# Kernel optimization log

Hardware: AMD Instinct MI355X
Metric: run time of the kernel (lower is better)

The kernel has to match this reference:

```python
import jax, jax.numpy as jnp
from jax import lax
import numpy as np
import math

KSIZE, STRIDE, RATE, FUSE_K, SCALE, FUSE = 3, 1, 2, 3, 10.0, True
DN = ('NCHW', 'OIHW', 'NCHW')


def extract_image_patches(img, kernel, stride=1):
    # Faithful to the torch helper, including the F.pad quirk where pad_row
    # (computed from height) is applied to the width axis and vice versa.
    bsz, c, h, w = img.shape
    h2 = math.ceil(h / stride)
    w2 = math.ceil(w / stride)
    pad_row = (h2 - 1) * stride + kernel - h
    pad_col = (w2 - 1) * stride + kernel - w
    x = jnp.pad(img, ((0, 0), (0, 0),
                      (pad_col // 2, pad_col - pad_col // 2),
                      (pad_row // 2, pad_row - pad_row // 2)))
    cols = []
    for i in range(kernel):
        for j in range(kernel):
            cols.append(x[:, :, i:i + (h2 - 1) * stride + 1:stride,
                          j:j + (w2 - 1) * stride + 1:stride])
    patches = jnp.stack(cols, axis=-1).reshape(bsz, c, h2, w2, kernel, kernel)
    patches = jnp.transpose(patches, (0, 4, 5, 1, 2, 3))  # [b,kh,kw,c,h2,w2]
    return patches.reshape(bsz, -1, h2, w2)


def setup_inputs() -> dict:
    key = jax.random.key(0)
    k1, k2, k3 = jax.random.split(key, 3)
    f = jax.random.normal(k1, (4, 128, 96, 96), dtype=jnp.float32)
    b = jax.random.normal(k2, (4, 128, 96, 96), dtype=jnp.float32)
    mask = jax.random.uniform(k3, (4, 1, 96, 96), dtype=jnp.float32)
    return {'f': f, 'b': b, 'mask': mask}


def reference(f, b, mask):
    bs, cs, hs, ws = f.shape
    kernel = RATE * 2
    # raw background patches used as conv_transpose filters (C-order reshape as in torch .view)
    raw_w = extract_image_patches(b, kernel, RATE * STRIDE)
    raw_w = raw_w.reshape(bs, -1, kernel, kernel, cs).transpose(0, 1, 4, 2, 3)  # [bs,L,cs,4,4]
    # nearest downsample by rate (matches F.interpolate nearest with scale 1/rate)
    fd = f[:, :, ::RATE, ::RATE]
    bd = b[:, :, ::RATE, ::RATE]
    md = mask[:, :, ::RATE, ::RATE]
    ih, iw = bd.shape[2], bd.shape[3]
    L = ih * iw
    w = extract_image_patches(bd, KSIZE, STRIDE)
    w = w.reshape(bs, -1, KSIZE, KSIZE, cs).transpose(0, 1, 4, 2, 3)  # [bs,L,cs,3,3]
    m = extract_image_patches(md, KSIZE, STRIDE)
    m = m.reshape(bs, -1, 1, KSIZE, KSIZE).transpose(0, 2, 3, 4, 1)  # [bs,1,3,3,L]
    mms = (jnp.mean(1.0 - m, axis=(1, 2, 3)) < 0.85).astype(f.dtype)  # [bs,L]
    fuse_w = jnp.eye(FUSE_K, dtype=f.dtype).reshape(1, 1, FUSE_K, FUSE_K)

    def per_sample(xi, wi, raw_wi, mm):
        # xi [cs,ih,iw], wi [L,cs,3,3], raw_wi [L,cs,4,4], mm [L]
        norm = jnp.sqrt(jnp.sum(wi * wi, axis=(1, 2, 3)) + 1e-8)
        wi_n = wi / jnp.maximum(norm, 1e-4)[:, None, None, None]
        yi = lax.conv_general_dilated(xi[None], wi_n, (1, 1), ((1, 1), (1, 1)),
                                      dimension_numbers=DN)  # [1,L,ih,iw]
        if FUSE:
            yi = yi.reshape(1, 1, ih * iw, ih * iw)
            yi = lax.conv_general_dilated(yi, fuse_w, (1, 1), ((1, 1), (1, 1)), dimension_numbers=DN)
            yi = yi.reshape(1, ih, iw, ih, iw).transpose(0, 2, 1, 4, 3)
            yi = yi.reshape(1, 1, ih * iw, ih * iw)
            yi = lax.conv_general_dilated(yi, fuse_w, (1, 1), ((1, 1), (1, 1)), dimension_numbers=DN)
            yi = yi.reshape(1, iw, ih, iw, ih).transpose(0, 2, 1, 4, 3)
        yi = yi.reshape(1, ih, iw, iw * ih)
        yi = yi * mm
        yi = jax.nn.softmax(yi * SCALE, axis=3)
        yi = yi * mm
        off = jnp.argmax(yi, axis=3).astype(jnp.int32)
        off = jnp.stack([off // hs, off % hs], axis=-1).transpose(0, 3, 1, 2)  # [1,2,ih,iw]
        yi = yi.transpose(0, 3, 1, 2)  # [1,L,ih,iw]
        # conv_transpose2d(yi, raw_wi, stride=RATE, padding=1) == dilated corr with flipped, transposed kernel
        w_t = jnp.flip(raw_wi, (-2, -1)).transpose(1, 0, 2, 3)  # [cs,L,4,4]
        pad = kernel - 1 - 1
        out = lax.conv_general_dilated(yi, w_t, (1, 1), ((pad, pad), (pad, pad)),
                                       lhs_dilation=(RATE, RATE), dimension_numbers=DN) / 4.0
        return out[0], off[0]

    y, offsets = jax.vmap(per_sample)(fd, w, raw_w, mms)  # y [bs,cs,hs,ws], offsets [bs,2,ih,iw]
    grid = jnp.stack([jnp.broadcast_to(jnp.arange(ih)[:, None], (ih, iw)),
                      jnp.broadcast_to(jnp.arange(iw)[None, :], (ih, iw))], 0).astype(jnp.int32)
    offsets = offsets - grid[None]
    # flow_to_image (external numpy visualization) omitted; raw offsets returned instead.
    return y, offsets
```

## Files before the change

### kernel.cpp

```cpp
#include <hip/hip_runtime.h>
#include <hip/hip_bf16.h>
#include <math.h>

#define IH 48
#define IW 48
#define LTOT 2304
#define CS 128
#define HS 96
#define KRED 1152
#define CRED 2048

typedef unsigned short u16;
typedef __attribute__((ext_vector_type(8))) short short8;
typedef __attribute__((ext_vector_type(8))) unsigned short ushort8;
typedef __attribute__((ext_vector_type(4))) float floatx4;

#define NS    ((size_t)LTOT*LTOT)
#define PLANE ((size_t)LTOT*KRED)

#define OFF_APL  ((size_t)0)
#define OFF_BPL  ((size_t)10616832)
#define OFF_S    ((size_t)21233664)
#define OFF_C    ((size_t)42467328)
#define OFF_SM   ((size_t)61341696)
#define REGION   ((size_t)61360128)

__device__ __forceinline__ u16 f2bf(float v) {
    __hip_bfloat16 h = __float2bfloat16(v);
    return *reinterpret_cast<u16*>(&h);
}
__device__ __forceinline__ float bf2f(u16 b) {
    __hip_bfloat16 h = *reinterpret_cast<__hip_bfloat16*>(&b);
    return __bfloat162float(h);
}
__device__ __forceinline__ void split2(float v, u16& a, u16& b) {
    a = f2bf(v);
    b = f2bf(v - bf2f(a));
}

__global__ __launch_bounds__(256) void k_wgather(const float* __restrict__ b,
                                                 u16* __restrict__ Ag,
                                                 int b0, size_t zsU) {
    int bi = b0 + blockIdx.z;
    u16* A = Ag + (size_t)blockIdx.z * zsU;
    int l = blockIdx.x, t = threadIdx.x;
    __shared__ float red[256];
    float myv[5];
    float ss = 0.f;
#pragma unroll
    for (int k = 0; k < 5; ++k) {
        int G = t + 256 * k;
        float val = 0.f;
        if (G < KRED) {
            int F = l * KRED + G;
            int p2 = F / LTOT, s = F - p2 * LTOT;
            int i = p2 / 384, j = (p2 / 128) % 3, c = p2 & 127;
            int u = s / IW + i - 1, v = s % IW + j - 1;
            if (u >= 0 && u < IH && v >= 0 && v < IW)
                val = b[(((size_t)bi * CS + c) * HS + 2 * u) * HS + 2 * v];
        }
        myv[k] = val;
        ss += val * val;
    }
    red[t] = ss; __syncthreads();
    for (int o = 128; o > 0; o >>= 1) { if (t < o) red[t] += red[t + o]; __syncthreads(); }
    float ninv = 1.0f / fmaxf(sqrtf(red[0] + 1e-8f), 1e-4f);
#pragma unroll
    for (int k = 0; k < 5; ++k) {
        int G = t + 256 * k;
        if (G < KRED) {
            u16 h1, h2; split2(myv[k] * ninv, h1, h2);
            size_t F = (size_t)l * KRED + G;
            A[F] = h1; A[PLANE + F] = h2;
        }
    }
}

__global__ __launch_bounds__(256) void k_gather_x_tiled(const float* __restrict__ f,
                                                        u16* __restrict__ Bg,
                                                        int b0, size_t zsU) {
    __shared__ float ldsf[128 * 55];
    int bi = b0 + blockIdx.z;
    u16* B = Bg + (size_t)blockIdx.z * zsU;
    int bx = blockIdx.x;
    int y = bx / 3, x0 = (bx % 3) * 16;
    int t = threadIdx.x;
    for (int i = 0; i < 27; ++i) {
        int g = i * 256 + t;
        if (g < 6912) {
            int vl = g % 18;
            int row = (g / 18) % 3;
            int c = g / 54;
            int u = y + row - 1;
            int v = x0 - 1 + vl;
            float val = 0.f;
            if (u >= 0 && u < IH && v >= 0 && v < IW)
                val = f[(((size_t)bi * CS + c) * HS + 2 * u) * HS + 2 * v];
            ldsf[c * 55 + row * 18 + vl] = val;
        }
    }
    __syncthreads();
    for (int i = 0; i < 72; ++i) {
        int o = i * 256 + t;
        int xp = o / 1152, G = o - xp * 1152;
        int k1 = G / 384, k2 = (G >> 7) % 3, c = G & 127;
        float val = ldsf[c * 55 + k1 * 18 + xp + k2];
        u16 h1, h2; split2(val, h1, h2);
        size_t idx = (size_t)(y * IW + x0 + xp) * KRED + G;
        B[idx] = h1; B[PLANE + idx] = h2;
    }
}

__global__ __launch_bounds__(256) void k_mm(const float* __restrict__ mask,
                                            float* __restrict__ mmvg, int b0, size_t zsF) {
    int bi = b0 + blockIdx.z;
    float* out = mmvg + (size_t)blockIdx.z * zsF;
    int q = blockIdx.x * 256 + threadIdx.x;
    if (q >= LTOT) return;
    float ssum = 0.f;
    for (int t = 0; t < 9; t++) {
        int F = q * 9 + t;
        int pm = F / LTOT, s = F % LTOT;
        int i = pm / 3, j = pm % 3;
        int u = s / IW + i - 1, v = s % IW + j - 1;
        float val = 0.f;
        if (u >= 0 && u < IH && v >= 0 && v < IW)
            val = mask[((size_t)bi * HS + 2 * u) * HS + 2 * v];
        ssum += 1.0f - val;
    }
    out[q] = (ssum / 9.0f < 0.85f) ? 1.0f : 0.0f;
}

template <int NP, int BK>
__global__ __launch_bounds__(256) void k_gemm_mfma(const u16* __restrict__ Ag,
                                                   const u16* __restrict__ Bg,
                                                   float* __restrict__ Cg,
                                                   size_t zsA, size_t zsB, size_t zsC,
                                                   size_t planeStride,
                                                   int M, int N, int K) {
    constexpr int SLOTS = BK / 8;
    constexpr int SMASK = SLOTS - 1;
    constexpr int TSZ = 128 * BK;
    constexpr int NLD = NP * BK / 16;
    __shared__ u16 lds[2 * NP * TSZ];
    u16* As = lds;
    u16* Bs = lds + NP * TSZ;
    const int tid = threadIdx.x;
    const int lane = tid & 63;
    const int wave = tid >> 6;
    const int wr = (wave >> 1) * 64, wc = (wave & 1) * 64;
    const int lrow = lane & 15, lq = lane >> 4;

    unsigned gx = gridDim.x, gy = gridDim.y;
    unsigned nwg = gx * gy * gridDim.z;
    unsigned wg = (blockIdx.z * gy + blockIdx.y) * gx + blockIdx.x;
    {
        unsigned q = nwg >> 3, r = nwg & 7, xcd = wg & 7, lid = wg >> 3;
        wg = (xcd < r ? xcd * (q + 1) : r * (q + 1) + (xcd - r) * q) + lid;
    }
    unsigned z = wg / (gx * gy);
    unsigned rem2 = wg - z * gx * gy;
    const int bm = (int)(rem2 / gx) * 128, bn = (int)(rem2 % gx) * 128;

    const u16* A = Ag + (size_t)z * zsA;
    const u16* B = Bg + (size_t)z * zsB;
    float* C = Cg + (size_t)z * zsC;

    floatx4 acc[4][4];
#pragma unroll
    for (int i = 0; i < 4; i++)
#pragma unroll
        for (int j = 0; j < 4; j++) acc[i][j] = (floatx4){0.f, 0.f, 0.f, 0.f};

    for (int kt = 0; kt < K; kt += BK) {
        ushort8 stA[NLD], stB[NLD];
#pragma unroll
        for (int e = 0; e < NLD; ++e) {
            int g = e * 256 + tid;
            int p = g / (128 * SLOTS);
            int gg = g % (128 * SLOTS);
            int row = gg / SLOTS, slot = gg & SMASK;
            stA[e] = *(const ushort8*)(A + (size_t)p * planeStride + (size_t)(bm + row) * K + kt + slot * 8);
            stB[e] = *(const ushort8*)(B + (size_t)p * planeStride + (size_t)(bn + row) * K + kt + slot * 8);
        }
        __syncthreads();
#pragma unroll
        for (int e = 0; e < NLD; ++e) {
            int g = e * 256 + tid;
            int p = g / (128 * SLOTS);
            int gg = g % (128 * SLOTS);
            int row = gg / SLOTS, slot = gg & SMASK;
            int dst = p * TSZ + row * BK + ((slot ^ (row & SMASK)) << 3);
            *(ushort8*)&As[dst] = stA[e];
            *(ushort8*)&Bs[dst] = stB[e];
        }
        __syncthreads();

#pragma unroll
        for (int ks = 0; ks < BK / 32; ++ks) {
            short8 af[NP][4];
#pragma unroll
            for (int p = 0; p < NP; ++p)
#pragma unroll
                for (int mi = 0; mi < 4; ++mi) {
                    int row = wr + mi * 16 + lrow;
                    af[p][mi] = *(const short8*)&As[p * TSZ + row * BK + ((((ks << 2) | lq) ^ (row & SMASK)) << 3)];
                }
#pragma unroll
            for (int ni = 0; ni < 4; ++ni) {
                short8 bfr[NP];
                int rowb = wc + ni * 16 + lrow;
                int bslot = ((((ks << 2) | lq) ^ (rowb & SMASK)) << 3);
#pragma unroll
                for (int p = 0; p < NP; ++p)
                    bfr[p] = *(const short8*)&Bs[p * TSZ + rowb * BK + bslot];
#pragma unroll
                for (int mi = 0; mi < 4; ++mi) {
                    if constexpr (NP == 1) {
                        acc[mi][ni] = __builtin_amdgcn_mfma_f32_16x16x32_bf16(af[0][mi], bfr[0], acc[mi][ni], 0, 0, 0);
                    } else {
                        acc[mi][ni] = __builtin_amdgcn_mfma_f32_16x16x32_bf16(af[1][mi], bfr[0], acc[mi][ni], 0, 0, 0);
                        acc[mi][ni] = __builtin_amdgcn_mfma_f32_16x16x32_bf16(af[0][mi], bfr[1], acc[mi][ni], 0, 0, 0);
                        acc[mi][ni] = __builtin_amdgcn_mfma_f32_16x16x32_bf16(af[0][mi], bfr[0], acc[mi][ni], 0, 0, 0);
                    }
                }
            }
        }
    }

    const int r0 = bm + wr + (lane >> 4) * 4;
    const int c0 = bn + wc + (lane & 15);
#pragma unroll
    for (int mi = 0; mi < 4; ++mi)
#pragma unroll
        for (int ni = 0; ni < 4; ++ni)
#pragma unroll
            for (int j = 0; j < 4; ++j)
                C[(size_t)(r0 + mi * 16 + j) * N + (c0 + ni * 16)] = acc[mi][ni][j];
}

__device__ __forceinline__ int permi(int a) { return (a % 48) * 48 + a / 48; }

__device__ __forceinline__ float f1_at(const float* __restrict__ S, int a, int b) {
    float s = S[(size_t)a * LTOT + b];
    if (a >= 1 && b >= 1) s += S[(size_t)(a - 1) * LTOT + (b - 1)];
    if (a < LTOT - 1 && b < LTOT - 1) s += S[(size_t)(a + 1) * LTOT + (b + 1)];
    return s;
}

__global__ __launch_bounds__(256) void k_fusesoftmax(const float* __restrict__ Sg,
                                                     const float* __restrict__ mmg,
                                                     const float* __restrict__ bsrc,
                                                     float* __restrict__ Cg,
                                                     float* __restrict__ offout,
                                                     int b0, size_t zsF) {
    int z = blockIdx.z;
    int bi = b0 + z;
    const float* S = Sg + (size_t)z * zsF;
    const float* mm = mmg + (size_t)z * zsF;
    float* C = Cg + (size_t)z * zsF;
    int bx = blockIdx.x;
    int l = (bx & 7) * 288 + (bx >> 3);
    int t = threadIdx.x;
    __shared__ float redv[256];
    __shared__ int redi[256];
    __shared__ int scand[2304];
    __shared__ float scv[2304];
    __shared__ int scnt;
    __shared__ int sAny;
    if (t == 0) { scnt = 0; sAny = 0; }

    const int At = permi(l);
    const int rm = (At >= 1) ? permi(At - 1) : -1;
    const int rp = (At < LTOT - 1) ? permi(At + 1) : -1;

    float v[9];
    bool mk[9];
    int nMaskLoc = 0;
#pragma unroll
    for (int i = 0; i < 9; ++i) {
        int p = t + 256 * i;
        float d = f1_at(S, l, p);
        if (rm >= 0 && p >= 1)
            d += f1_at(S, rm, (p >= 48) ? p - 48 : 2255 + p);
        if (rp >= 0 && p != 2303)
            d += f1_at(S, rp, (p < 2256) ? p + 48 : p - 2255);
        float m = mm[p];
        mk[i] = (m > 0.f);
        if (!mk[i]) nMaskLoc++;
        v[i] = d * m * 10.0f;
    }
    float lmu = -1e30f; int lidx = 0x7fffffff;
#pragma unroll
    for (int i = 0; i < 9; ++i) {
        int p = t + 256 * i;
        if (mk[i] && v[i] > lmu) { lmu = v[i]; lidx = p; }
    }
    if (nMaskLoc) sAny = 1;
    redv[t] = lmu; redi[t] = lidx; __syncthreads();
    for (int o = 128; o > 0; o >>= 1) {
        if (t < o) {
            if (redv[t + o] > redv[t] || (redv[t + o] == redv[t] && redi[t + o] < redi[t])) {
                redv[t] = redv[t + o]; redi[t] = redi[t + o];
            }
        }
        __syncthreads();
    }
    float mu = redv[0];
    int muIdx = redi[0];
    int anyM = sAny;
    __syncthreads();
    redi[t] = nMaskLoc; __syncthreads();
    for (int o = 128; o > 0; o >>= 1) { if (t < o) redi[t] += redi[t + o]; __syncthreads(); }
    int nMask = redi[0];
    __syncthreads();

    float mx = anyM ? fmaxf(mu, 0.f) : mu;

#pragma unroll
    for (int i = 0; i < 9; ++i) {
        int p = t + 256 * i;
        if (mk[i] && v[i] >= mu - 20.0f) {
            int pos = atomicAdd(&scnt, 1);
            scand[pos] = p;
            scv[pos] = v[i];
        }
    }
    __syncthreads();
    int cnt = scnt;

    float Z = (float)nMask * __expf(0.f - mx);
    for (int ci = 0; ci < cnt; ++ci) Z += __expf(scv[ci] - mx);

    if (t == 0) {
        int bestp = (cnt > 0) ? muIdx : 0;
        int ly = l / IW, lx = l % IW;
        offout[((size_t)bi * 2 + 0) * LTOT + l] = (float)(bestp / 96 - ly);
        offout[((size_t)bi * 2 + 1) * LTOT + l] = (float)(bestp % 96 - lx);
    }

    float accv[8];
#pragma unroll
    for (int j = 0; j < 8; ++j) accv[j] = 0.f;
    for (int ci = 0; ci < cnt; ++ci) {
        int p = scand[ci];
        float w = __expf(scv[ci] - mx) / Z;
        int F0 = p * 2048 + t;
        int pr = F0 / 2304;
        int s = F0 - pr * 2304;
        int srow = s / 48;
        int scol = s - srow * 48;
#pragma unroll
        for (int j = 0; j < 8; ++j) {
            int ii = pr >> 9, jj = (pr >> 7) & 3, c = pr & 127;
            int Y0 = 2 * srow + ii - 1, X0 = 2 * scol + jj - 1;
            float val = 0.f;
            if (Y0 >= 0 && Y0 < HS && X0 >= 0 && X0 < HS)
                val = bsrc[(((size_t)bi * CS + c) * HS + Y0) * HS + X0];
            accv[j] += w * val;
            scol += 16; if (scol >= 48) { scol -= 48; srow += 1; }
            srow += 5;
            s += 256; if (s >= 2304) { s -= 2304; pr += 1; srow -= 48; }
        }
    }
    float* Crow = C + (size_t)l * CRED;
#pragma unroll
    for (int j = 0; j < 8; ++j) Crow[t + 256 * j] = accv[j] * 0.25f;
}

__global__ __launch_bounds__(256) void k_output_tiled(const float* __restrict__ Cg,
                                                      float* __restrict__ yout,
                                                      int b0, size_t zsF) {
    __shared__ float lo[64 * 129];
    int bi = b0 + blockIdx.z;
    const float* C = Cg + (size_t)blockIdx.z * zsF;
    int bx = blockIdx.x;
    int Y0 = (bx / 6) * 4, X0 = (bx % 6) * 16;
    int t = threadIdx.x;
    int c = t & 127;
    for (int i = 0; i < 32; ++i) {
        int pos = i * 2 + (t >> 7);
        int Y = Y0 + (pos >> 4), X = X0 + (pos & 15);
        float s = 0.f;
        int pu = (Y + 1) & 1, pv = (X + 1) & 1;
#pragma unroll
        for (int a = 0; a < 2; a++) {
            int u = pu + 2 * a;
            int ly2 = Y + 1 - u;
            if (ly2 < 0) continue;
            int ly = ly2 >> 1;
            if (ly >= IH) continue;
#pragma unroll
            for (int bb = 0; bb < 2; bb++) {
                int v = pv + 2 * bb;
                int lx2 = X + 1 - v;
                if (lx2 < 0) continue;
                int lx = lx2 >> 1;
                if (lx >= IW) continue;
                s += C[(size_t)(ly * IW + lx) * CRED + u * 512 + v * 128 + c];
            }
        }
        lo[pos * 129 + c] = s;
    }
    __syncthreads();
    for (int i = 0; i < 32; ++i) {
        int cc = i * 4 + (t >> 6);
        int pos = t & 63;
        float val = lo[pos * 129 + cc];
        int yl = pos >> 4, xl = pos & 15;
        yout[(((size_t)bi * CS + cc) * HS + Y0 + yl) * HS + X0 + xl] = val;
    }
}

extern "C" void kernel_launch(void* const* d_in, const int* in_sizes, int n_in,
                              void* d_out, int out_size, void* d_ws, size_t ws_size,
                              hipStream_t stream) {
    const float* f = (const float*)d_in[0];
    const float* b = (const float*)d_in[1];
    const float* mask = (const float*)d_in[2];
    float* yout = (float*)d_out;
    float* offout = yout + (size_t)4 * CS * HS * HS;

    int ZB, nloop;
    if (ws_size >= 4 * REGION)      { ZB = 4; nloop = 1; }
    else if (ws_size >= 2 * REGION) { ZB = 2; nloop = 2; }
    else                            { ZB = 1; nloop = 4; }

    char* base = (char*)d_ws;
    u16*   Apl  = (u16*)(base + OFF_APL);
    u16*   Bpl  = (u16*)(base + OFF_BPL);
    float* S    = (float*)(base + OFF_S);
    float* Cc   = (float*)(base + OFF_C);
    float* mmv  = (float*)(base + OFF_SM);

    const size_t zsU = REGION / 2;
    const size_t zsF = REGION / 4;

    dim3 blk(256, 1, 1);

    for (int it = 0; it < nloop; ++it) {
        int b0 = it * ZB;
        k_wgather<<<dim3(LTOT, 1, ZB), blk, 0, stream>>>(b, Apl, b0, zsU);
        k_gather_x_tiled<<<dim3(IH * 3, 1, ZB), blk, 0, stream>>>(f, Bpl, b0, zsU);
        k_mm<<<dim3((LTOT + 255) / 256, 1, ZB), blk, 0, stream>>>(mask, mmv, b0, zsF);
        k_gemm_mfma<2, 64><<<dim3(LTOT / 128, LTOT / 128, ZB), blk, 0, stream>>>(
            Apl, Bpl, S, zsU, zsU, zsF, PLANE, LTOT, LTOT, KRED);
        k_fusesoftmax<<<dim3(LTOT, 1, ZB), blk, 0, stream>>>(S, mmv, b, Cc, offout, b0, zsF);
        k_output_tiled<<<dim3((HS / 4) * (HS / 16), 1, ZB), blk, 0, stream>>>(Cc, yout, b0, zsF);
    }
}
```

Measured before the change: 474.7 us.

## Split fuse step into diagonal sliding-window pass, border pass, and softmax kernel

The 9-tap fuse sum that was computed inside the softmax kernel through scattered permuted-index loads now has its own kernels. A diagonal-strip kernel walks each diagonal with a register sliding window, so every S element is loaded once instead of nine times. A separate border kernel handles the wrap-around rows and columns. The softmax kernel then reads one precomputed row. This adds a full LTOT×LTOT intermediate V buffer write and read plus two extra launches, and reuses the S region for C to make room for V.

```diff
diff --git a/kernel.cpp b/kernel.cpp
--- a/kernel.cpp
+++ b/kernel.cpp
@@ -21,9 +21,9 @@
 #define OFF_APL  ((size_t)0)
 #define OFF_BPL  ((size_t)10616832)
 #define OFF_S    ((size_t)21233664)
-#define OFF_C    ((size_t)42467328)
-#define OFF_SM   ((size_t)61341696)
-#define REGION   ((size_t)61360128)
+#define OFF_V    ((size_t)42467328)
+#define OFF_SM   ((size_t)63700992)
+#define REGION   ((size_t)63719424)
 
 __device__ __forceinline__ u16 f2bf(float v) {
     __hip_bfloat16 h = __float2bfloat16(v);
@@ -239,29 +239,97 @@
                 C[(size_t)(r0 + mi * 16 + j) * N + (c0 + ni * 16)] = acc[mi][ni][j];
 }
 
-__device__ __forceinline__ int permi(int a) { return (a % 48) * 48 + a / 48; }
-
-__device__ __forceinline__ float f1_at(const float* __restrict__ S, int a, int b) {
-    float s = S[(size_t)a * LTOT + b];
-    if (a >= 1 && b >= 1) s += S[(size_t)(a - 1) * LTOT + (b - 1)];
-    if (a < LTOT - 1 && b < LTOT - 1) s += S[(size_t)(a + 1) * LTOT + (b + 1)];
-    return s;
-}
-
-__global__ __launch_bounds__(256) void k_fusesoftmax(const float* __restrict__ Sg,
-                                                     const float* __restrict__ mmg,
-                                                     const float* __restrict__ bsrc,
-                                                     float* __restrict__ Cg,
-                                                     float* __restrict__ offout,
-                                                     int b0, size_t zsF) {
+#define SEG 192
+__global__ __launch_bounds__(256) void k_fuse_diag(const float* __restrict__ Sg,
+                                                   float* __restrict__ Vg,
+                                                   size_t zsF) {
+    int z = blockIdx.z;
+    const float* S = Sg + (size_t)z * zsF;
+    float* V = Vg + (size_t)z * zsF;
+    int t = threadIdx.x;
+    int dstrip = blockIdx.x % 18;
+    int seg = blockIdx.x / 18;
+    int delta = dstrip * 256 + t - 2303;
+    int kmin = delta < 0 ? -delta : 0;
+    int kmax = delta > 0 ? LTOT - delta : LTOT;
+    int hiC = (kmax - 1 > kmin) ? kmax - 1 : kmin;
+    const int s0 = seg * SEG;
+
+#define GLOAD(idx) ({                                            \
+    int _i = (idx);                                              \
+    int _c = _i < kmin ? kmin : (_i > hiC ? hiC : _i);           \
+    float _x = S[(size_t)_c * (LTOT + 1) + delta];               \
+    (_i >= kmin && _i < kmax) ? _x : 0.f; })
+
+    float old0 = GLOAD(s0 - 49), old1 = GLOAD(s0 - 48), old2 = GLOAD(s0 - 47);
+    float mid0 = GLOAD(s0 - 1),  mid1 = GLOAD(s0),      mid2 = GLOAD(s0 + 1);
+    float rec0 = GLOAD(s0 + 47), rec1 = GLOAD(s0 + 48), rec2 = GLOAD(s0 + 49);
+
+    for (int kp = s0; kp < s0 + SEG; ++kp) {
+        float v = ((old0 + old1) + (old2 + mid0)) + ((mid1 + mid2) + (rec0 + rec1)) + rec2;
+        if (kp >= kmin && kp < kmax)
+            V[(size_t)kp * (LTOT + 1) + delta] = v;
+        old0 = old1; old1 = old2; old2 = GLOAD(kp - 46);
+        mid0 = mid1; mid1 = mid2; mid2 = GLOAD(kp + 2);
+        rec0 = rec1; rec1 = rec2; rec2 = GLOAD(kp + 50);
+    }
+#undef GLOAD
+}
+
+__global__ __launch_bounds__(256) void k_fuse_border(const float* __restrict__ Sg,
+                                                     float* __restrict__ Vg,
+                                                     size_t zsF) {
+    int z = blockIdx.z;
+    const float* S = Sg + (size_t)z * zsF;
+    float* V = Vg + (size_t)z * zsF;
+    int e = blockIdx.x * 256 + threadIdx.x;
+    int l, p;
+    if (e < 96 * LTOT) {
+        int lb = e / LTOT;
+        l = (lb < 48) ? lb : lb + 2208;
+        p = e - lb * LTOT;
+    } else {
+        int e2 = e - 96 * LTOT;
+        int r = e2 / 96;
+        l = 48 + r;
+        int po = e2 - r * 96;
+        p = (po < 48) ? po : po + 2208;
+    }
+    const bool hasRm = (l >= 1), hasRp = (l < 2303);
+    const int rm = (l >= 48) ? l - 48 : 2255 + l;
+    const int rp = (l < 2256) ? l + 48 : l - 2255;
+    const bool cm = (p >= 1), cp = (p < 2303);
+    const int pm = (p >= 48) ? p - 48 : 2255 + p;
+    const int pp = (p < 2256) ? p + 48 : p - 2255;
+
+    float d = S[(size_t)l * LTOT + p];
+    if (hasRm && cm) d += S[(size_t)(l - 1) * LTOT + (p - 1)];
+    if (hasRp && cp) d += S[(size_t)(l + 1) * LTOT + (p + 1)];
+    if (hasRm && cm) {
+        d += S[(size_t)rm * LTOT + pm];
+        if (rm >= 1 && pm >= 1)       d += S[(size_t)(rm - 1) * LTOT + (pm - 1)];
+        if (rm < 2303 && pm < 2303)   d += S[(size_t)(rm + 1) * LTOT + (pm + 1)];
+    }
+    if (hasRp && cp) {
+        d += S[(size_t)rp * LTOT + pp];
+        if (rp >= 1 && pp >= 1)       d += S[(size_t)(rp - 1) * LTOT + (pp - 1)];
+        if (rp < 2303 && pp < 2303)   d += S[(size_t)(rp + 1) * LTOT + (pp + 1)];
+    }
+    V[(size_t)l * LTOT + p] = d;
+}
+
+__global__ __launch_bounds__(256) void k_softmaxC(const float* __restrict__ Vg,
+                                                  const float* __restrict__ mmg,
+                                                  const float* __restrict__ bsrc,
+                                                  float* __restrict__ Cg,
+                                                  float* __restrict__ offout,
+                                                  int b0, size_t zsF) {
     int z = blockIdx.z;
     int bi = b0 + z;
-    const float* S = Sg + (size_t)z * zsF;
+    const float* Vr = Vg + (size_t)z * zsF;
     const float* mm = mmg + (size_t)z * zsF;
     float* C = Cg + (size_t)z * zsF;
-    int bx = blockIdx.x;
-    int l = (bx & 7) * 288 + (bx >> 3);
-    int t = threadIdx.x;
+    int l = blockIdx.x, t = threadIdx.x;
     __shared__ float redv[256];
     __shared__ int redi[256];
     __shared__ int scand[2304];
@@ -270,25 +338,17 @@
     __shared__ int sAny;
     if (t == 0) { scnt = 0; sAny = 0; }
 
-    const int At = permi(l);
-    const int rm = (At >= 1) ? permi(At - 1) : -1;
-    const int rp = (At < LTOT - 1) ? permi(At + 1) : -1;
-
+    const float* row = Vr + (size_t)l * LTOT;
     float v[9];
     bool mk[9];
     int nMaskLoc = 0;
 #pragma unroll
     for (int i = 0; i < 9; ++i) {
         int p = t + 256 * i;
-        float d = f1_at(S, l, p);
-        if (rm >= 0 && p >= 1)
-            d += f1_at(S, rm, (p >= 48) ? p - 48 : 2255 + p);
-        if (rp >= 0 && p != 2303)
-            d += f1_at(S, rp, (p < 2256) ? p + 48 : p - 2255);
         float m = mm[p];
         mk[i] = (m > 0.f);
         if (!mk[i]) nMaskLoc++;
-        v[i] = d * m * 10.0f;
+        v[i] = row[p] * m * 10.0f;
     }
     float lmu = -1e30f; int lidx = 0x7fffffff;
 #pragma unroll
@@ -430,7 +490,8 @@
     u16*   Apl  = (u16*)(base + OFF_APL);
     u16*   Bpl  = (u16*)(base + OFF_BPL);
     float* S    = (float*)(base + OFF_S);
-    float* Cc   = (float*)(base + OFF_C);
+    float* Cc   = (float*)(base + OFF_S);
+    float* V    = (float*)(base + OFF_V);
     float* mmv  = (float*)(base + OFF_SM);
 
     const size_t zsU = REGION / 2;
@@ -445,7 +506,9 @@
         k_mm<<<dim3((LTOT + 255) / 256, 1, ZB), blk, 0, stream>>>(mask, mmv, b0, zsF);
         k_gemm_mfma<2, 64><<<dim3(LTOT / 128, LTOT / 128, ZB), blk, 0, stream>>>(
             Apl, Bpl, S, zsU, zsU, zsF, PLANE, LTOT, LTOT, KRED);
-        k_fusesoftmax<<<dim3(LTOT, 1, ZB), blk, 0, stream>>>(S, mmv, b, Cc, offout, b0, zsF);
+        k_fuse_diag<<<dim3(18 * (LTOT / SEG), 1, ZB), blk, 0, stream>>>(S, V, zsF);
+        k_fuse_border<<<dim3(1692, 1, ZB), blk, 0, stream>>>(S, V, zsF);
+        k_softmaxC<<<dim3(LTOT, 1, ZB), blk, 0, stream>>>(V, mmv, b, Cc, offout, b0, zsF);
         k_output_tiled<<<dim3((HS / 4) * (HS / 16), 1, ZB), blk, 0, stream>>>(Cc, yout, b0, zsF);
     }
 }
```

After: 672.7 us. +41.7%, slower.
